# Optimization experiments

Measured on AMD Instinct MI355X. Metric: run time of the kernel, lower is better.

The kernel has to match this reference:

```python
import jax, jax.numpy as jnp
import numpy as np

UNITS = 512
M = 8
INPUT_DIM = 512
BATCH = 2048


def setup_inputs() -> dict:
    key = jax.random.key(0)
    ks = jax.random.split(key, 9)
    D, U = INPUT_DIM, UNITS
    fused_dim = D + U
    def glorot(k, shape):
        lim = np.sqrt(6.0 / (shape[0] + shape[1])).astype(np.float32)
        return jax.random.uniform(k, shape, jnp.float32, -lim, lim)
    return {
        "inputs": jax.random.normal(ks[0], (BATCH, D), jnp.float32),
        "elapsed": jax.random.uniform(ks[1], (BATCH, 1), jnp.float32),
        "state": jax.random.normal(ks[2], (BATCH, U * M), jnp.float32),
        "W_r": glorot(ks[3], (fused_dim, U * M)),
        "b_r": jnp.zeros((U * M,), jnp.float32),
        "W_d": glorot(ks[4], (fused_dim, U)),
        "b_d": jnp.zeros((U,), jnp.float32),
        "W_u": glorot(ks[5], (fused_dim, U * M)),
        "b_u": jnp.zeros((U * M,), jnp.float32),
    }


def reference(inputs, elapsed, state, W_r, b_r, W_d, b_d, W_u, b_u):
    B = inputs.shape[0]
    # tau_i = 10**(i/2)  =>  ln_tau_i = i * 0.5 * ln(10)
    ln_tau_table = 0.5 * jnp.log(jnp.float32(10.0)) * jnp.arange(M, dtype=jnp.float32)  # [M]
    tau_table = jnp.exp(ln_tau_table)  # [M]

    h_hat = state.reshape(B, UNITS, M)            # [B, U, M]
    h = h_hat.sum(axis=2)                          # [B, U]
    fused = jnp.concatenate([inputs, h], axis=-1)  # [B, D+U]

    # retrieval gate: softmax over M buckets of -(ln_tau_r - table)^2
    ln_tau_r = (fused @ W_r + b_r).reshape(B, UNITS, M)
    rki = jax.nn.softmax(-jnp.square(ln_tau_r - ln_tau_table), axis=2)
    q_input = jnp.sum(rki * h_hat, axis=2)         # [B, U]

    # detect (candidate) with tanh
    reset_value = jnp.concatenate([inputs, q_input], axis=1)
    qk = jnp.tanh(reset_value @ W_d + b_d)[:, :, None]  # [B, U, 1]

    # update gate
    ln_tau_s = (fused @ W_u + b_u).reshape(B, UNITS, M)
    ski = jax.nn.softmax(-jnp.square(ln_tau_s - ln_tau_table), axis=2)

    # exponential decay per bucket: elapsed [B,1] / tau [M] -> [B, M]
    exp_term = jnp.exp(-elapsed / tau_table)[:, None, :]  # [B, 1, M]
    h_hat_next = ((1.0 - ski) * h_hat + ski * qk) * exp_term  # [B, U, M]

    h_next = h_hat_next.sum(axis=2)                # [B, U]
    return h_next, h_hat_next.reshape(B, UNITS * M)
```

## Files before the change

kernel.cpp:

```cpp
#include <hip/hip_runtime.h>
#include <hip/hip_fp16.h>
#include <cmath>

#define B_SZ 2048
#define D_IN 512
#define U_N  512
#define FD   1024
#define NRU  4096
#define NRU2 8192

typedef _Float16 f16x8 __attribute__((ext_vector_type(8)));
typedef float    f32x4 __attribute__((ext_vector_type(4)));

typedef const __attribute__((address_space(1))) void glb_cv;
typedef __attribute__((address_space(3))) void lds_v;

#define TAB_INIT {0.0f, 1.15129254649702f, 2.30258509299405f, \
                  3.45387763949107f, 4.60517018598809f, 5.75646273248511f, \
                  6.90775527898214f, 8.05904782547916f}

__global__ __launch_bounds__(256) void prep_kernel(
    const float* __restrict__ inputs, const float* __restrict__ state,
    __half* __restrict__ fused, __half* __restrict__ reset)
{
    const int b = blockIdx.x;
    const int t = threadIdx.x;

    const float2 iv = *(const float2*)(inputs + (size_t)b * D_IN + t * 2);
    __half2 hv;
    hv.x = __float2half(iv.x);
    hv.y = __float2half(iv.y);
    *(__half2*)(fused + (size_t)b * FD + t * 2) = hv;
    *(__half2*)(reset + (size_t)b * FD + t * 2) = hv;

    const float4* sp = (const float4*)(state + (size_t)b * NRU + t * 16);
    float4 x0 = sp[0], x1 = sp[1], x2 = sp[2], x3 = sp[3];
    float s0 = (x0.x + x0.y) + (x0.z + x0.w) + (x1.x + x1.y) + (x1.z + x1.w);
    float s1 = (x2.x + x2.y) + (x2.z + x2.w) + (x3.x + x3.y) + (x3.z + x3.w);
    __half2 h2;
    h2.x = __float2half(s0);
    h2.y = __float2half(s1);
    *(__half2*)(fused + (size_t)b * FD + D_IN + t * 2) = h2;
}

__global__ __launch_bounds__(256) void convT3_kernel(
    const float* __restrict__ W_r, const float* __restrict__ W_u,
    const float* __restrict__ W_d, __half* __restrict__ WruT,
    __half* __restrict__ WdT)
{
    __shared__ float tile[32][33];
    const int bx = blockIdx.x;
    const float* W;
    __half* Wt;
    int N, nt;
    if (bx < 128)      { W = W_r; Wt = WruT;                    N = NRU; nt = bx * 32; }
    else if (bx < 256) { W = W_u; Wt = WruT + (size_t)NRU * FD; N = NRU; nt = (bx - 128) * 32; }
    else               { W = W_d; Wt = WdT;                     N = U_N; nt = (bx - 256) * 32; }

    const int kt = blockIdx.y * 32;
    const int t  = threadIdx.x;
    const int c  = t & 31;
    const int r4 = t >> 5;

#pragma unroll
    for (int i = 0; i < 4; i++) {
        int r = r4 + i * 8;
        tile[r][c] = W[(size_t)(kt + r) * N + nt + c];
    }
    __syncthreads();
#pragma unroll
    for (int i = 0; i < 4; i++) {
        int rr = r4 + i * 8;
        Wt[(size_t)(nt + rr) * FD + kt + c] = __float2half(tile[c][rr]);
    }
}

__global__ __launch_bounds__(512, 2) void gemm_big(
    const __half* __restrict__ A, const __half* __restrict__ Bt,
    const float* __restrict__ b_r, const float* __restrict__ b_u,
    const float* __restrict__ state, __half* __restrict__ resetw,
    __half* __restrict__ skibuf)
{
    __shared__ __align__(16) char smem[131072];
    __half* SAh = (__half*)smem;

    const int t    = threadIdx.x;
    const int m0   = blockIdx.y << 8;
    const int n0   = blockIdx.x << 8;
    const int lane = t & 63;
    const int w    = t >> 6;
    const int wm16 = ((w >> 2) & 1) << 4;
    const int wn16 = (w & 3) << 4;
    const int m16  = lane & 15;
    const int quad = lane >> 4;
    const int g0   = (quad ^ (m16 & 7)) << 3;
    const int g1   = ((quad + 4) ^ (m16 & 7)) << 3;
    const int t8   = t << 3;
    const int trow = t >> 3;
    const int gcol = ((t & 7) ^ (trow & 7)) << 3;

    const __half* gA = A  + (size_t)(m0 + trow) * FD + gcol;
    const __half* gB = Bt + (size_t)(n0 + trow) * FD + gcol;

    f32x4 acc[8][4];
#pragma unroll
    for (int a1 = 0; a1 < 8; a1++)
#pragma unroll
        for (int a2 = 0; a2 < 4; a2++)
            acc[a1][a2] = (f32x4){0.f, 0.f, 0.f, 0.f};

#define BARRIER() __builtin_amdgcn_s_barrier()
#define PRIO1 __builtin_amdgcn_s_setprio(1)
#define PRIO0 __builtin_amdgcn_s_setprio(0)
#define WAITV(n) do { asm volatile("s_waitcnt vmcnt(" #n ")" ::: "memory"); \
                      __builtin_amdgcn_sched_barrier(0); } while (0)
#define WAITL() do { asm volatile("s_waitcnt lgkmcnt(0)" ::: "memory"); \
                     __builtin_amdgcn_sched_barrier(0); } while (0)

#define STAGE_A(buf, h, tt) do { \
        const __half* _s = gA + (size_t)((h) * 128) * FD + (tt) * 64; \
        __half* _d = SAh + (buf) * 32768 + (h) * 8192 + t8; \
        __builtin_amdgcn_global_load_lds((glb_cv*)_s, (lds_v*)_d, 16, 0, 0); \
        __builtin_amdgcn_global_load_lds((glb_cv*)(_s + (size_t)64 * FD), \
                                         (lds_v*)(_d + 4096), 16, 0, 0); } while (0)
#define STAGE_B(buf, h, tt) do { \
        const __half* _s = gB + (size_t)((h) * 128) * FD + (tt) * 64; \
        __half* _d = SAh + (buf) * 32768 + 16384 + (h) * 8192 + t8; \
        __builtin_amdgcn_global_load_lds((glb_cv*)_s, (lds_v*)_d, 16, 0, 0); \
        __builtin_amdgcn_global_load_lds((glb_cv*)(_s + (size_t)64 * FD), \
                                         (lds_v*)(_d + 4096), 16, 0, 0); } while (0)

#define READ_A(c, mh) do { _Pragma("unroll") \
    for (int mi2 = 0; mi2 < 4; mi2++) { \
        const __half* _ap = SAh + (c) * 32768 + \
            ((((mh) * 4 + mi2) * 32 + wm16 + m16) << 6); \
        af[mi2][0] = *(const f16x8*)(_ap + g0); \
        af[mi2][1] = *(const f16x8*)(_ap + g1); } } while (0)
#define READ_B(c, nh) do { _Pragma("unroll") \
    for (int ni2 = 0; ni2 < 2; ni2++) { \
        const __half* _bp = SAh + (c) * 32768 + 16384 + \
            ((((nh) * 2 + ni2) * 64 + wn16 + m16) << 6); \
        bf[ni2][0] = *(const f16x8*)(_bp + g0); \
        bf[ni2][1] = *(const f16x8*)(_bp + g1); } } while (0)

#define MFMAQ(MH, NH) do { _Pragma("unroll") \
    for (int mi2 = 0; mi2 < 4; mi2++) { _Pragma("unroll") \
        for (int ni2 = 0; ni2 < 2; ni2++) { \
            acc[(MH)*4+mi2][(NH)*2+ni2] = __builtin_amdgcn_mfma_f32_16x16x32_f16( \
                af[mi2][0], bf[ni2][0], acc[(MH)*4+mi2][(NH)*2+ni2], 0, 0, 0); \
            acc[(MH)*4+mi2][(NH)*2+ni2] = __builtin_amdgcn_mfma_f32_16x16x32_f16( \
                af[mi2][1], bf[ni2][1], acc[(MH)*4+mi2][(NH)*2+ni2], 0, 0, 0); } } } while (0)

    STAGE_A(0, 0, 0); STAGE_B(0, 0, 0); STAGE_A(0, 1, 0); STAGE_B(0, 1, 0);
    STAGE_A(1, 0, 1); STAGE_B(1, 1, 1); STAGE_A(1, 1, 1);
    WAITV(6);
    BARRIER();

#pragma unroll 1
    for (int i = 0; i < 8; i++) {
        const int ta = (2 * i + 1) & 15, tb = (2 * i + 2) & 15, tc = (2 * i + 3) & 15;
        f16x8 af[4][2], bf[2][2];
        READ_A(0, 0); READ_B(0, 0); STAGE_B(1, 0, ta);
        BARRIER(); WAITL(); PRIO1; MFMAQ(0, 0); PRIO0; BARRIER();
        READ_B(0, 1); STAGE_A(0, 0, tb);
        BARRIER(); WAITL(); PRIO1; MFMAQ(0, 1); PRIO0; BARRIER();
        READ_A(0, 1); STAGE_B(0, 1, tb);
        BARRIER(); WAITL(); PRIO1; MFMAQ(1, 1); PRIO0; BARRIER();
        READ_B(0, 0); STAGE_A(0, 1, tb);
        BARRIER(); WAITL(); PRIO1; MFMAQ(1, 0); PRIO0; WAITV(6); BARRIER();
        READ_A(1, 0); READ_B(1, 0); STAGE_B(0, 0, tb);
        BARRIER(); WAITL(); PRIO1; MFMAQ(0, 0); PRIO0; BARRIER();
        READ_B(1, 1); STAGE_A(1, 0, tc);
        BARRIER(); WAITL(); PRIO1; MFMAQ(0, 1); PRIO0; BARRIER();
        READ_A(1, 1); STAGE_B(1, 1, tc);
        BARRIER(); WAITL(); PRIO1; MFMAQ(1, 1); PRIO0; BARRIER();
        READ_B(1, 0); STAGE_A(1, 1, tc);
        BARRIER(); WAITL(); PRIO1; MFMAQ(1, 0); PRIO0; WAITV(6); BARRIER();
    }

    WAITV(0);
    __syncthreads();

#undef BARRIER
#undef PRIO1
#undef PRIO0
#undef WAITV
#undef WAITL
#undef STAGE_A
#undef STAGE_B
#undef READ_A
#undef READ_B
#undef MFMAQ

    float*  ebuf = (float*)smem;
    __half* qbuf = (__half*)(smem + 256 * 68 * 4);
    const bool is_r = (n0 < NRU);
    const float* bp = is_r ? b_r : b_u;
    const int n0r = is_r ? n0 : n0 - NRU;
    const float TAB[8] = TAB_INIT;

    for (int ni = 0; ni < 4; ni++) {
        const float bv = bp[n0r + ni * 64 + wn16 + m16];
#pragma unroll
        for (int mi = 0; mi < 8; mi++)
#pragma unroll
            for (int r = 0; r < 4; r++)
                ebuf[(mi * 32 + wm16 + quad * 4 + r) * 68 + wn16 + m16] =
                    acc[mi][ni][r] + bv;
        __syncthreads();

#pragma unroll
        for (int p = 0; p < 4; p++) {
            const int item = p * 512 + t;
            const int row = item >> 3, g = item & 7;
            const int b = m0 + row;
            const float* rp = ebuf + row * 68 + g * 8;
            float v[8];
            *(float4*)&v[0] = *(const float4*)rp;
            *(float4*)&v[4] = *(const float4*)(rp + 4);

            float e[8], sum = 0.f;
#pragma unroll
            for (int i2 = 0; i2 < 8; i2++) {
                float d = v[i2] - TAB[i2];
                e[i2] = __expf(-d * d);
                sum += e[i2];
            }
            const int colr = n0r + ni * 64 + g * 8;
            if (is_r) {
                const float4 h0 = *(const float4*)(state + (size_t)b * NRU + colr);
                const float4 h1 = *(const float4*)(state + (size_t)b * NRU + colr + 4);
                const float hv[8] = {h0.x, h0.y, h0.z, h0.w, h1.x, h1.y, h1.z, h1.w};
                float qn = 0.f;
#pragma unroll
                for (int i2 = 0; i2 < 8; i2++) qn += e[i2] * hv[i2];
                qbuf[row * 8 + g] = __float2half(qn / sum);
            } else {
                const float inv = 1.0f / sum;
                __half2 o[4];
#pragma unroll
                for (int i2 = 0; i2 < 4; i2++) {
                    o[i2].x = __float2half(e[2 * i2] * inv);
                    o[i2].y = __float2half(e[2 * i2 + 1] * inv);
                }
                *(uint4*)(skibuf + (size_t)b * NRU + colr) = *(uint4*)o;
            }
        }
        __syncthreads();
        if (is_r) {
            const int row = t >> 1, lg = (t & 1) << 2;
            uint2 qv = *(uint2*)(qbuf + row * 8 + lg);
            *(uint2*)(resetw + (size_t)(m0 + row) * FD + D_IN + (n0r >> 3) + ni * 8 + lg) = qv;
        }
    }
}

template <int BM, int EPI>
__global__ __launch_bounds__(256) void gemm_k(
    const __half* __restrict__ A, const __half* __restrict__ Bt,
    const float* __restrict__ biasA, const float* __restrict__ biasB, int nsplit,
    float* __restrict__ C, int Ncols,
    const float* __restrict__ state, __half* __restrict__ resetw,
    __half* __restrict__ skibuf, int K)
{
    extern __shared__ __align__(16) char smem[];
    __half* sA = (__half*)smem;
    __half* sB = (__half*)(smem + BM * 128);

    const int t    = threadIdx.x;
    const int m0   = blockIdx.y * BM;
    const int n0   = blockIdx.x << 7;
    const int lane = t & 63;
    const int w    = t >> 6;
    const int m16  = lane & 15;
    const int quad = lane >> 4;
    constexpr int MI = BM / 32;
    constexpr int IA = BM / 32;
    const int wm = (w & 1) * (BM / 2);
    const int wn = (w >> 1) << 6;

    f32x4 acc[MI][4];
#pragma unroll
    for (int i = 0; i < MI; i++)
#pragma unroll
        for (int j = 0; j < 4; j++)
#pragma unroll
            for (int r = 0; r < 4; r++) acc[i][j][r] = 0.f;

    const __half* gAp[IA];
    const __half* lAp[IA];
#pragma unroll
    for (int i = 0; i < IA; i++) {
        const int off = w * (BM * 32) + i * 1024 + lane * 16;
        const int row = off >> 7;
        const int g   = ((off & 127) >> 4) ^ (row & 7);
        gAp[i] = A + (size_t)(m0 + row) * K + g * 8;
        lAp[i] = sA + ((w * (BM * 32) + i * 1024) >> 1);
    }
    const __half* gBp[4];
    const __half* lBp[4];
#pragma unroll
    for (int i = 0; i < 4; i++) {
        const int off = w * 4096 + i * 1024 + lane * 16;
        const int row = off >> 7;
        const int g   = ((off & 127) >> 4) ^ (row & 7);
        gBp[i] = Bt + (size_t)(n0 + row) * K + g * 8;
        lBp[i] = sB + ((w * 4096 + i * 1024) >> 1);
    }

    for (int kt = 0; kt < K; kt += 64) {
        __syncthreads();
#pragma unroll
        for (int i = 0; i < IA; i++)
            __builtin_amdgcn_global_load_lds((glb_cv*)(gAp[i] + kt), (lds_v*)lAp[i], 16, 0, 0);
#pragma unroll
        for (int i = 0; i < 4; i++)
            __builtin_amdgcn_global_load_lds((glb_cv*)(gBp[i] + kt), (lds_v*)lBp[i], 16, 0, 0);
        __syncthreads();

#pragma unroll
        for (int s = 0; s < 2; s++) {
            f16x8 af[MI], bf[4];
#pragma unroll
            for (int mi = 0; mi < MI; mi++) {
                const int row = wm + mi * 16 + m16;
                const int gi  = (s * 4 + quad) ^ (row & 7);
                af[mi] = *(const f16x8*)(sA + row * 64 + gi * 8);
            }
#pragma unroll
            for (int ni = 0; ni < 4; ni++) {
                const int row = wn + ni * 16 + m16;
                const int gi  = (s * 4 + quad) ^ (row & 7);
                bf[ni] = *(const f16x8*)(sB + row * 64 + gi * 8);
            }
#pragma unroll
            for (int mi = 0; mi < MI; mi++)
#pragma unroll
                for (int ni = 0; ni < 4; ni++)
                    acc[mi][ni] = __builtin_amdgcn_mfma_f32_16x16x32_f16(
                        af[mi], bf[ni], acc[mi][ni], 0, 0, 0);
        }
    }

    if constexpr (EPI == 0) {
#pragma unroll
        for (int mi = 0; mi < MI; mi++) {
#pragma unroll
            for (int ni = 0; ni < 4; ni++) {
                const int col = n0 + wn + ni * 16 + m16;
                const float bv = biasA[col];
#pragma unroll
                for (int r = 0; r < 4; r++) {
                    const int row = m0 + wm + mi * 16 + quad * 4 + r;
                    C[(size_t)row * Ncols + col] = tanhf(acc[mi][ni][r] + bv);
                }
            }
        }
    }
}

__global__ __launch_bounds__(256) void final_kernel(
    const __half* __restrict__ skibuf, const float* __restrict__ state,
    const float* __restrict__ qk, const float* __restrict__ elapsed,
    float* __restrict__ out0, float* __restrict__ out1)
{
    const int idx = blockIdx.x * 256 + threadIdx.x;
    const int b = idx >> 9;
    const int u = idx & 511;

    const float INV_TAU[8] = {1.0f, 0.316227766016838f, 0.1f, 0.0316227766016838f,
                              0.01f, 0.00316227766016838f, 0.001f, 0.000316227766016838f};

    const uint4 sr = *(const uint4*)(skibuf + (size_t)b * NRU + u * 8);
    const __half2* sh = (const __half2*)&sr;
    float sk[8];
#pragma unroll
    for (int i = 0; i < 4; i++) {
        float2 f2 = __half22float2(sh[i]);
        sk[2 * i]     = f2.x;
        sk[2 * i + 1] = f2.y;
    }

    const float4* hh = (const float4*)(state + ((size_t)b * NRU + u * 8));
    float4 h0 = hh[0], h1 = hh[1];
    float h[8] = {h0.x, h0.y, h0.z, h0.w, h1.x, h1.y, h1.z, h1.w};

    const float q  = qk[(size_t)b * U_N + u];
    const float el = elapsed[b];

    float hn[8];
    float acc = 0.f;
#pragma unroll
    for (int i = 0; i < 8; i++) {
        const float et = __expf(-el * INV_TAU[i]);
        hn[i] = ((1.0f - sk[i]) * h[i] + sk[i] * q) * et;
        acc += hn[i];
    }

    float4* o = (float4*)(out1 + ((size_t)b * NRU + u * 8));
    o[0] = make_float4(hn[0], hn[1], hn[2], hn[3]);
    o[1] = make_float4(hn[4], hn[5], hn[6], hn[7]);
    out0[(size_t)b * U_N + u] = acc;
}

extern "C" void kernel_launch(void* const* d_in, const int* in_sizes, int n_in,
                              void* d_out, int out_size, void* d_ws, size_t ws_size,
                              hipStream_t stream)
{
    (void)in_sizes; (void)n_in; (void)out_size; (void)ws_size;

    const float* inputs  = (const float*)d_in[0];
    const float* elapsed = (const float*)d_in[1];
    const float* state   = (const float*)d_in[2];
    const float* W_r     = (const float*)d_in[3];
    const float* b_r     = (const float*)d_in[4];
    const float* W_d     = (const float*)d_in[5];
    const float* b_d     = (const float*)d_in[6];
    const float* W_u     = (const float*)d_in[7];
    const float* b_u     = (const float*)d_in[8];
    float* out = (float*)d_out;

    char* ws = (char*)d_ws;
    __half* fused  = (__half*)(ws);
    __half* reset  = (__half*)(ws + ((size_t)4  << 20));
    __half* WruT   = (__half*)(ws + ((size_t)8  << 20));
    __half* WdT    = (__half*)(ws + ((size_t)24 << 20));
    __half* skibuf = (__half*)(ws + ((size_t)25 << 20));
    float*  qk     = (float*) (ws + ((size_t)41 << 20));

    prep_kernel<<<B_SZ, 256, 0, stream>>>(inputs, state, fused, reset);
    convT3_kernel<<<dim3(272, FD / 32), 256, 0, stream>>>(W_r, W_u, W_d, WruT, WdT);

    gemm_big<<<dim3(NRU2 / 256, B_SZ / 256), 512, 0, stream>>>(
        fused, WruT, b_r, b_u, state, reset, skibuf);

    gemm_k<64, 0><<<dim3(U_N / 128, B_SZ / 64), 256, 24576, stream>>>(
        reset, WdT, b_d, nullptr, 1 << 30, qk, U_N, nullptr, nullptr, nullptr, FD);

    final_kernel<<<(B_SZ * U_N) / 256, 256, 0, stream>>>(skibuf, state, qk, elapsed, out,
                                                         out + (size_t)B_SZ * U_N);
}
```

Measured before the change: 200.3 us.

## Restructure GEMM main loop to four phases with full B fragment reuse

The main MFMA loop moves from eight quarter-tile phases, each reading half of B, to four phases in which all B fragments are loaded once per k-step and reused across two A halves. The global-to-LDS staging order and the vmcnt wait thresholds are reworked to match. The aim is fewer barriers and fewer redundant LDS reads per k-step. In exchange each wave holds more B-fragment registers, and the prefetch distance for some stages is shorter, which could expose load latency.

```diff
diff --git a/kernel.cpp b/kernel.cpp
--- a/kernel.cpp
+++ b/kernel.cpp
@@ -136,46 +136,43 @@
             ((((mh) * 4 + mi2) * 32 + wm16 + m16) << 6); \
         af[mi2][0] = *(const f16x8*)(_ap + g0); \
         af[mi2][1] = *(const f16x8*)(_ap + g1); } } while (0)
-#define READ_B(c, nh) do { _Pragma("unroll") \
-    for (int ni2 = 0; ni2 < 2; ni2++) { \
+#define READ_B_ALL(c) do { _Pragma("unroll") \
+    for (int ni2 = 0; ni2 < 4; ni2++) { \
         const __half* _bp = SAh + (c) * 32768 + 16384 + \
-            ((((nh) * 2 + ni2) * 64 + wn16 + m16) << 6); \
+            ((ni2 * 64 + wn16 + m16) << 6); \
         bf[ni2][0] = *(const f16x8*)(_bp + g0); \
         bf[ni2][1] = *(const f16x8*)(_bp + g1); } } while (0)
 
-#define MFMAQ(MH, NH) do { _Pragma("unroll") \
+#define MFMA_Q(MH) do { _Pragma("unroll") \
     for (int mi2 = 0; mi2 < 4; mi2++) { _Pragma("unroll") \
-        for (int ni2 = 0; ni2 < 2; ni2++) { \
-            acc[(MH)*4+mi2][(NH)*2+ni2] = __builtin_amdgcn_mfma_f32_16x16x32_f16( \
-                af[mi2][0], bf[ni2][0], acc[(MH)*4+mi2][(NH)*2+ni2], 0, 0, 0); \
-            acc[(MH)*4+mi2][(NH)*2+ni2] = __builtin_amdgcn_mfma_f32_16x16x32_f16( \
-                af[mi2][1], bf[ni2][1], acc[(MH)*4+mi2][(NH)*2+ni2], 0, 0, 0); } } } while (0)
-
-    STAGE_A(0, 0, 0); STAGE_B(0, 0, 0); STAGE_A(0, 1, 0); STAGE_B(0, 1, 0);
-    STAGE_A(1, 0, 1); STAGE_B(1, 1, 1); STAGE_A(1, 1, 1);
-    WAITV(6);
+        for (int ni2 = 0; ni2 < 4; ni2++) { \
+            acc[(MH)*4+mi2][ni2] = __builtin_amdgcn_mfma_f32_16x16x32_f16( \
+                af[mi2][0], bf[ni2][0], acc[(MH)*4+mi2][ni2], 0, 0, 0); \
+            acc[(MH)*4+mi2][ni2] = __builtin_amdgcn_mfma_f32_16x16x32_f16( \
+                af[mi2][1], bf[ni2][1], acc[(MH)*4+mi2][ni2], 0, 0, 0); } } } while (0)
+
+    STAGE_B(0, 0, 0); STAGE_B(0, 1, 0);
+    STAGE_A(0, 0, 0); STAGE_A(0, 1, 0);
+    STAGE_B(1, 0, 1); STAGE_B(1, 1, 1);
+    WAITV(4);
     BARRIER();
 
 #pragma unroll 1
     for (int i = 0; i < 8; i++) {
-        const int ta = (2 * i + 1) & 15, tb = (2 * i + 2) & 15, tc = (2 * i + 3) & 15;
-        f16x8 af[4][2], bf[2][2];
-        READ_A(0, 0); READ_B(0, 0); STAGE_B(1, 0, ta);
-        BARRIER(); WAITL(); PRIO1; MFMAQ(0, 0); PRIO0; BARRIER();
-        READ_B(0, 1); STAGE_A(0, 0, tb);
-        BARRIER(); WAITL(); PRIO1; MFMAQ(0, 1); PRIO0; BARRIER();
-        READ_A(0, 1); STAGE_B(0, 1, tb);
-        BARRIER(); WAITL(); PRIO1; MFMAQ(1, 1); PRIO0; BARRIER();
-        READ_B(0, 0); STAGE_A(0, 1, tb);
-        BARRIER(); WAITL(); PRIO1; MFMAQ(1, 0); PRIO0; WAITV(6); BARRIER();
-        READ_A(1, 0); READ_B(1, 0); STAGE_B(0, 0, tb);
-        BARRIER(); WAITL(); PRIO1; MFMAQ(0, 0); PRIO0; BARRIER();
-        READ_B(1, 1); STAGE_A(1, 0, tc);
-        BARRIER(); WAITL(); PRIO1; MFMAQ(0, 1); PRIO0; BARRIER();
-        READ_A(1, 1); STAGE_B(1, 1, tc);
-        BARRIER(); WAITL(); PRIO1; MFMAQ(1, 1); PRIO0; BARRIER();
-        READ_B(1, 0); STAGE_A(1, 1, tc);
-        BARRIER(); WAITL(); PRIO1; MFMAQ(1, 0); PRIO0; WAITV(6); BARRIER();
+        const int t1 = (2 * i + 1) & 15, t2 = (2 * i + 2) & 15, t3 = (2 * i + 3) & 15;
+        f16x8 af[4][2], bf[4][2];
+        READ_B_ALL(0); READ_A(0, 0);
+        STAGE_A(1, 0, t1); STAGE_A(1, 1, t1);
+        BARRIER(); WAITL(); PRIO1; MFMA_Q(0); PRIO0; BARRIER();
+        READ_A(0, 1);
+        STAGE_B(0, 0, t2); STAGE_B(0, 1, t2);
+        BARRIER(); WAITL(); PRIO1; MFMA_Q(1); PRIO0; WAITV(4); BARRIER();
+        READ_B_ALL(1); READ_A(1, 0);
+        STAGE_A(0, 0, t2); STAGE_A(0, 1, t2);
+        BARRIER(); WAITL(); PRIO1; MFMA_Q(0); PRIO0; BARRIER();
+        READ_A(1, 1);
+        STAGE_B(1, 0, t3); STAGE_B(1, 1, t3);
+        BARRIER(); WAITL(); PRIO1; MFMA_Q(1); PRIO0; WAITV(4); BARRIER();
     }
 
     WAITV(0);
@@ -189,8 +186,8 @@
 #undef STAGE_A
 #undef STAGE_B
 #undef READ_A
-#undef READ_B
-#undef MFMAQ
+#undef READ_B_ALL
+#undef MFMA_Q
 
     float*  ebuf = (float*)smem;
     __half* qbuf = (__half*)(smem + 256 * 68 * 4);
```

Result: no change. 200.1 us (-0.1%).
